# Optimization experiments

Measured on AMD Instinct MI355X. Metric: run time of the kernel, lower is better.

Reference implementation:

```python
import jax, jax.numpy as jnp
import numpy as np

SPATIAL_SHAPES = ((100, 167), (50, 84), (25, 42), (13, 21))
NUM_HEADS = 8
NUM_LEVELS = 4
NUM_POINTS = 4
EMBED_DIM = 256
LV = sum(h * w for h, w in SPATIAL_SHAPES)  # 22223


def bilinear_sample(img, grid):
    """torch.F.grid_sample(mode='bilinear', padding_mode='zeros', align_corners=False).
    img: (B, D, H, W); grid: (B, Lq, P, 2) with xy in [-1, 1]. Returns (B, D, Lq, P)."""
    B, D, H, W = img.shape
    x = (grid[..., 0] + 1.0) * 0.5 * W - 0.5  # (B, Lq, P)
    y = (grid[..., 1] + 1.0) * 0.5 * H - 0.5
    x0 = jnp.floor(x)
    y0 = jnp.floor(y)
    wx1 = x - x0
    wy1 = y - y0
    wx0 = 1.0 - wx1
    wy0 = 1.0 - wy1

    def gather(ix, iy):
        valid = ((ix >= 0) & (ix <= W - 1) & (iy >= 0) & (iy <= H - 1)).astype(img.dtype)
        ixc = jnp.clip(ix, 0, W - 1).astype(jnp.int32)
        iyc = jnp.clip(iy, 0, H - 1).astype(jnp.int32)

        def g(img_b, ixb, iyb, vb):
            return img_b[:, iyb, ixb] * vb[None]  # (D, Lq, P)

        return jax.vmap(g)(img, ixc, iyc, valid)  # (B, D, Lq, P)

    v00 = gather(x0, y0)
    v01 = gather(x0 + 1, y0)
    v10 = gather(x0, y0 + 1)
    v11 = gather(x0 + 1, y0 + 1)
    w00 = (wy0 * wx0)[:, None]
    w01 = (wy0 * wx1)[:, None]
    w10 = (wy1 * wx0)[:, None]
    w11 = (wy1 * wx1)[:, None]
    return v00 * w00 + v01 * w01 + v10 * w10 + v11 * w11


def deform_attn(query, ref_points, value, W_off, b_off, W_attn, b_attn, W_val, b_val, W_out, b_out):
    N, Lq, C = query.shape
    D = C // NUM_HEADS
    off = (query @ W_off + b_off).reshape(N, Lq, NUM_HEADS, NUM_LEVELS, NUM_POINTS, 2)
    attn = jax.nn.softmax((query @ W_attn + b_attn).reshape(N, Lq, NUM_HEADS, NUM_LEVELS * NUM_POINTS), axis=-1)
    attn = attn.reshape(N, Lq, NUM_HEADS, NUM_LEVELS, NUM_POINTS)
    ref_cxcy = ref_points[:, :, None, :, None, :2]
    ref_wh = ref_points[:, :, None, :, None, 2:]
    loc = ref_cxcy + off / NUM_POINTS * ref_wh * 0.5
    grids = 2.0 * loc - 1.0  # (N, Lq, nh, L, P, 2)

    v = value @ W_val + b_val  # (N, Lv, C)
    sampled = []
    start = 0
    for lvl, (H, W) in enumerate(SPATIAL_SHAPES):
        v_l = v[:, start:start + H * W]  # (N, HW, C)
        start += H * W
        v_l = v_l.transpose(0, 2, 1).reshape(N * NUM_HEADS, D, H, W)
        g_l = grids[:, :, :, lvl].transpose(0, 2, 1, 3, 4).reshape(N * NUM_HEADS, Lq, NUM_POINTS, 2)
        sampled.append(bilinear_sample(v_l, g_l))  # (N*nh, D, Lq, P)
    sampled = jnp.concatenate(sampled, axis=-1)  # (N*nh, D, Lq, L*P)

    attn_r = attn.transpose(0, 2, 1, 3, 4).reshape(N * NUM_HEADS, 1, Lq, NUM_LEVELS * NUM_POINTS)
    out = (sampled * attn_r).sum(-1)  # (N*nh, D, Lq)
    out = out.reshape(N, C, Lq).transpose(0, 2, 1)
    return out @ W_out + b_out


def setup_inputs() -> dict:
    key = jax.random.key(0)
    ks = jax.random.split(key, 8)
    N, Lq, C = 1, LV, EMBED_DIM
    s = 0.02
    return {
        "query": jax.random.normal(ks[0], (N, Lq, C), jnp.float32),
        "ref_points": jax.random.uniform(ks[1], (N, Lq, NUM_LEVELS, 4), jnp.float32),
        "value": jax.random.normal(ks[2], (N, LV, C), jnp.float32),
        "W_off": jax.random.normal(ks[3], (C, NUM_HEADS * NUM_LEVELS * NUM_POINTS * 2), jnp.float32) * s,
        "b_off": jnp.zeros((NUM_HEADS * NUM_LEVELS * NUM_POINTS * 2,), jnp.float32),
        "W_attn": jax.random.normal(ks[4], (C, NUM_HEADS * NUM_LEVELS * NUM_POINTS), jnp.float32) * s,
        "b_attn": jnp.zeros((NUM_HEADS * NUM_LEVELS * NUM_POINTS,), jnp.float32),
        "W_val": jax.random.normal(ks[5], (C, C), jnp.float32) * s,
        "b_val": jnp.zeros((C,), jnp.float32),
        "W_out": jax.random.normal(ks[6], (C, C), jnp.float32) * s,
        "b_out": jnp.zeros((C,), jnp.float32),
    }


def reference(query, ref_points, value, W_off, b_off, W_attn, b_attn, W_val, b_val, W_out, b_out):
    return deform_attn(query, ref_points, value, W_off, b_off, W_attn, b_attn, W_val, b_val, W_out, b_out)
```

## Files before the change

kernel.cpp:

```cpp
#include <hip/hip_runtime.h>
#include <math.h>

#define LQ 22223
#define NH 8
#define NL 4
#define NP 4
#define CDIM 256
#define MBLK 348
#define NBV  (176 * 8)
#define NBOA (264 * 8)

typedef __attribute__((ext_vector_type(8))) short short8;
typedef __attribute__((ext_vector_type(4))) float f32x4;

__device__ __forceinline__ ushort f2bf(float f) {
    union { float f; unsigned u; } c; c.f = f;
    unsigned u = c.u;
    return (ushort)((u + 0x7fffu + ((u >> 16) & 1u)) >> 16);
}
__device__ __forceinline__ float bflo(unsigned u) {
    union { unsigned u; float f; } c; c.u = u << 16; return c.f;
}
__device__ __forceinline__ float bfhi(unsigned u) {
    union { unsigned u; float f; } c; c.u = u & 0xffff0000u; return c.f;
}

__global__ __launch_bounds__(256) void convert_wt(
    const float* __restrict__ Wv, const float* __restrict__ Wo,
    const float* __restrict__ Wu, const float* __restrict__ Wa,
    const float* __restrict__ bo, const float* __restrict__ ba,
    ushort* __restrict__ Tv, ushort* __restrict__ Toa,
    ushort* __restrict__ Tu, float* __restrict__ bcat)
{
    int idx = blockIdx.x * 256 + threadIdx.x;
    if (idx >= 229376) {
        int b = idx - 229376;
        if (b < 384) bcat[b] = (b < 256) ? bo[b] : ba[b - 256];
        return;
    }
    const float* W; ushort* T; int N; int local;
    if      (idx < 65536)  { W = Wv; T = Tv;          N = 256; local = idx; }
    else if (idx < 131072) { W = Wo; T = Toa;         N = 256; local = idx - 65536; }
    else if (idx < 196608) { W = Wu; T = Tu;          N = 256; local = idx - 131072; }
    else                   { W = Wa; T = Toa + 65536; N = 128; local = idx - 196608; }
    int k = local & 255;
    int n = local >> 8;
    T[n * 256 + k] = f2bf(W[k * N + n]);
}

__global__ __launch_bounds__(256, 5) void gemm_dual(
    const float* __restrict__ value, const ushort* __restrict__ Wtv,
    const float* __restrict__ bv, ushort* __restrict__ Cv,
    const float* __restrict__ query, const ushort* __restrict__ Wtoa,
    const float* __restrict__ boa, float* __restrict__ Coa)
{
    const int K = 256;
    __shared__ ushort As[2][64 * 40];
    __shared__ ushort Bs[2][64 * 40];

    int b = blockIdx.x;
    const float* A; const ushort* Bt; const float* bias;
    int N, bx, by; bool isv;
    const int xcd = b & 7;
    if (b < NBV) {
        isv = true;  A = value; Bt = Wtv;  bias = bv;  N = 256;
        const int j = b >> 3;
        bx = j & 3;  by = xcd + 8 * (j >> 2);
    } else {
        isv = false; A = query; Bt = Wtoa; bias = boa; N = 384;
        const int j = (b - NBV) >> 3;
        bx = j % 6;  by = xcd + 8 * (j / 6);
    }
    if (by >= MBLK) return;

    const int tid = threadIdx.x;
    const int w = tid >> 6;
    const int l = tid & 63;
    const int bm = by * 64;
    const int bn = bx * 64;

    const int r = tid >> 2;
    const int c = tid & 3;

    const int m_l  = (w << 4) + (l & 15);
    const int koff = (l >> 4) << 3;

    const bool arow_ok = (bm + r) < LQ;
    const float*  Ap = A  + (size_t)(bm + r) * K + c * 8;
    const ushort* Bp = Bt + (size_t)(bn + r) * K + c * 8;

    auto ldA = [&](int k0) -> short8 {
        short8 av = {0, 0, 0, 0, 0, 0, 0, 0};
        if (arow_ok) {
            const float4 f0 = *reinterpret_cast<const float4*>(Ap + k0);
            const float4 f1 = *reinterpret_cast<const float4*>(Ap + k0 + 4);
            av[0] = (short)f2bf(f0.x); av[1] = (short)f2bf(f0.y);
            av[2] = (short)f2bf(f0.z); av[3] = (short)f2bf(f0.w);
            av[4] = (short)f2bf(f1.x); av[5] = (short)f2bf(f1.y);
            av[6] = (short)f2bf(f1.z); av[7] = (short)f2bf(f1.w);
        }
        return av;
    };

    short8 av = ldA(0);
    short8 bvv = *reinterpret_cast<const short8*>(Bp);
    *reinterpret_cast<short8*>(&As[0][r * 40 + c * 8]) = av;
    *reinterpret_cast<short8*>(&Bs[0][r * 40 + c * 8]) = bvv;

    f32x4 acc[4] = {};

    #pragma unroll
    for (int k = 0; k < 8; ++k) {
        __syncthreads();
        if (k < 7) {
            av  = ldA((k + 1) * 32);
            bvv = *reinterpret_cast<const short8*>(Bp + (k + 1) * 32);
        }
        const int cur = k & 1;
        const short8 af = *reinterpret_cast<const short8*>(&As[cur][m_l * 40 + koff]);
        #pragma unroll
        for (int t = 0; t < 4; ++t) {
            const short8 bf = *reinterpret_cast<const short8*>(
                &Bs[cur][(t * 16 + (l & 15)) * 40 + koff]);
            acc[t] = __builtin_amdgcn_mfma_f32_16x16x32_bf16(af, bf, acc[t], 0, 0, 0);
        }
        if (k < 7) {
            const int nxt = cur ^ 1;
            *reinterpret_cast<short8*>(&As[nxt][r * 40 + c * 8]) = av;
            *reinterpret_cast<short8*>(&Bs[nxt][r * 40 + c * 8]) = bvv;
        }
    }

    const int row0 = bm + (w << 4) + ((l >> 4) << 2);
    #pragma unroll
    for (int t = 0; t < 4; ++t) {
        const int col = bn + t * 16 + (l & 15);
        const float bs = bias[col];
        #pragma unroll
        for (int i = 0; i < 4; ++i) {
            const int row = row0 + i;
            if (row < LQ) {
                const float o = acc[t][i] + bs;
                if (isv) Cv[(size_t)row * 256 + col] = f2bf(o);
                else     Coa[(size_t)row * 384 + col] = o;
            }
        }
    }
}

__global__ __launch_bounds__(256, 5) void gemm_out(
    const ushort* __restrict__ A, const ushort* __restrict__ Bt,
    const float* __restrict__ bias, float* __restrict__ C)
{
    const int K = 256, N = 256;
    __shared__ ushort As[2][64 * 40];
    __shared__ ushort Bs[2][64 * 40];

    const int b = blockIdx.x;
    const int xcd = b & 7;
    const int j = b >> 3;
    const int bx = j & 3;
    const int by = xcd + 8 * (j >> 2);
    if (by >= MBLK) return;

    const int tid = threadIdx.x;
    const int w = tid >> 6;
    const int l = tid & 63;
    const int bm = by * 64;
    const int bn = bx * 64;

    const int r = tid >> 2;
    const int c = tid & 3;

    const int m_l  = (w << 4) + (l & 15);
    const int koff = (l >> 4) << 3;

    const bool arow_ok = (bm + r) < LQ;
    const ushort* Ap = A  + (size_t)(bm + r) * K + c * 8;
    const ushort* Bp = Bt + (size_t)(bn + r) * K + c * 8;

    auto ldA = [&](int k0) -> short8 {
        short8 av = {0, 0, 0, 0, 0, 0, 0, 0};
        if (arow_ok) av = *reinterpret_cast<const short8*>(Ap + k0);
        return av;
    };

    short8 av = ldA(0);
    short8 bvv = *reinterpret_cast<const short8*>(Bp);
    *reinterpret_cast<short8*>(&As[0][r * 40 + c * 8]) = av;
    *reinterpret_cast<short8*>(&Bs[0][r * 40 + c * 8]) = bvv;

    f32x4 acc[4] = {};

    #pragma unroll
    for (int k = 0; k < 8; ++k) {
        __syncthreads();
        if (k < 7) {
            av  = ldA((k + 1) * 32);
            bvv = *reinterpret_cast<const short8*>(Bp + (k + 1) * 32);
        }
        const int cur = k & 1;
        const short8 af = *reinterpret_cast<const short8*>(&As[cur][m_l * 40 + koff]);
        #pragma unroll
        for (int t = 0; t < 4; ++t) {
            const short8 bf = *reinterpret_cast<const short8*>(
                &Bs[cur][(t * 16 + (l & 15)) * 40 + koff]);
            acc[t] = __builtin_amdgcn_mfma_f32_16x16x32_bf16(af, bf, acc[t], 0, 0, 0);
        }
        if (k < 7) {
            const int nxt = cur ^ 1;
            *reinterpret_cast<short8*>(&As[nxt][r * 40 + c * 8]) = av;
            *reinterpret_cast<short8*>(&Bs[nxt][r * 40 + c * 8]) = bvv;
        }
    }

    const int row0 = bm + (w << 4) + ((l >> 4) << 2);
    #pragma unroll
    for (int t = 0; t < 4; ++t) {
        const int col = bn + t * 16 + (l & 15);
        const float bs = bias[col];
        #pragma unroll
        for (int i = 0; i < 4; ++i) {
            const int row = row0 + i;
            if (row < LQ) C[(size_t)row * N + col] = acc[t][i] + bs;
        }
    }
}

__global__ __launch_bounds__(256) void softmax16(float* __restrict__ offattn, int rows)
{
    const int r = blockIdx.x * 256 + threadIdx.x;
    if (r >= rows) return;
    const int q = r >> 3;
    const int h = r & 7;
    float4* p = reinterpret_cast<float4*>(offattn + (size_t)q * 384 + 256 + h * 16);
    float v[16];
    #pragma unroll
    for (int i = 0; i < 4; ++i) {
        const float4 f = p[i];
        v[i * 4 + 0] = f.x; v[i * 4 + 1] = f.y; v[i * 4 + 2] = f.z; v[i * 4 + 3] = f.w;
    }
    float m = v[0];
    #pragma unroll
    for (int i = 1; i < 16; ++i) m = fmaxf(m, v[i]);
    float s = 0.f;
    #pragma unroll
    for (int i = 0; i < 16; ++i) { v[i] = expf(v[i] - m); s += v[i]; }
    const float inv = 1.f / s;
    #pragma unroll
    for (int i = 0; i < 4; ++i)
        p[i] = make_float4(v[i * 4 + 0] * inv, v[i * 4 + 1] * inv,
                           v[i * 4 + 2] * inv, v[i * 4 + 3] * inv);
}

__global__ __launch_bounds__(256, 5) void msda_sample(
    const ushort* __restrict__ v, const float* __restrict__ offattn,
    const float* __restrict__ ref, ushort* __restrict__ outp)
{
    __shared__ int4   s_off[1024];
    __shared__ float4 s_wts[1024];

    const int h = blockIdx.x & 7;
    const int qbase = (blockIdx.x >> 3) * 64;
    const int tid = threadIdx.x;

    const int Hs[4] = {100, 50, 25, 13};
    const int Ws[4] = {167, 84, 42, 21};
    const int starts[4] = {0, 16700, 20900, 21950};
    const int h32 = h * 32;

    #pragma unroll
    for (int t2 = 0; t2 < 4; ++t2) {
        const int t = t2 * 256 + tid;
        const int qi = t & 63;
        const int pi = t >> 6;
        const int q = qbase + qi;
        if (q < LQ) {
            const int l = pi >> 2;
            const int W = Ws[l], H = Hs[l];
            const float* refq = ref + (size_t)q * (NL * 4) + l * 4;
            const float cx = refq[0], cy = refq[1], rw = refq[2], rh = refq[3];
            const float* row = offattn + (size_t)q * 384;
            const float ox  = row[h32 + pi * 2];
            const float oy  = row[h32 + pi * 2 + 1];
            const float wgt = row[256 + h * 16 + pi];

            const float lx = cx + ox * 0.125f * rw;
            const float ly = cy + oy * 0.125f * rh;
            const float x = lx * (float)W - 0.5f;
            const float y = ly * (float)H - 0.5f;

            const float x0f = floorf(x);
            const float y0f = floorf(y);
            const int x0 = (int)x0f, y0 = (int)y0f;
            const float wx1 = x - x0f, wy1 = y - y0f;
            const float wx0 = 1.f - wx1, wy0 = 1.f - wy1;

            const bool xv0 = (x0 >= 0) && (x0 < W);
            const bool xv1 = (x0 + 1 >= 0) && (x0 + 1 < W);
            const bool yv0 = (y0 >= 0) && (y0 < H);
            const bool yv1 = (y0 + 1 >= 0) && (y0 + 1 < H);

            const int x0c = min(max(x0, 0), W - 1);
            const int x1c = min(max(x0 + 1, 0), W - 1);
            const int y0c = min(max(y0, 0), H - 1);
            const int y1c = min(max(y0 + 1, 0), H - 1);

            int4 ob;
            ob.x = ((starts[l] + y0c * W + x0c) << 8) + h32;
            ob.y = ((starts[l] + y0c * W + x1c) << 8) + h32;
            ob.z = ((starts[l] + y1c * W + x0c) << 8) + h32;
            ob.w = ((starts[l] + y1c * W + x1c) << 8) + h32;
            float4 wb;
            wb.x = (xv0 && yv0) ? wgt * wy0 * wx0 : 0.f;
            wb.y = (xv1 && yv0) ? wgt * wy0 * wx1 : 0.f;
            wb.z = (xv0 && yv1) ? wgt * wy1 * wx0 : 0.f;
            wb.w = (xv1 && yv1) ? wgt * wy1 * wx1 : 0.f;
            s_off[t] = ob;
            s_wts[t] = wb;
        }
    }
    __syncthreads();

    const int qi = tid >> 2;
    const int dg = tid & 3;
    const int q = qbase + qi;
    if (q >= LQ) return;
    const int d8 = dg * 8;

    float acc[8] = {};

    #pragma unroll 4
    for (int p = 0; p < 16; ++p) {
        const int4   o = s_off[p * 64 + qi];
        const float4 w = s_wts[p * 64 + qi];
        const uint4 a0 = *reinterpret_cast<const uint4*>(v + o.x + d8);
        const uint4 a1 = *reinterpret_cast<const uint4*>(v + o.y + d8);
        const uint4 a2 = *reinterpret_cast<const uint4*>(v + o.z + d8);
        const uint4 a3 = *reinterpret_cast<const uint4*>(v + o.w + d8);
        const unsigned u0[4] = {a0.x, a0.y, a0.z, a0.w};
        const unsigned u1[4] = {a1.x, a1.y, a1.z, a1.w};
        const unsigned u2[4] = {a2.x, a2.y, a2.z, a2.w};
        const unsigned u3[4] = {a3.x, a3.y, a3.z, a3.w};
        #pragma unroll
        for (int j = 0; j < 4; ++j) {
            acc[2 * j]     += w.x * bflo(u0[j]) + w.y * bflo(u1[j])
                            + w.z * bflo(u2[j]) + w.w * bflo(u3[j]);
            acc[2 * j + 1] += w.x * bfhi(u0[j]) + w.y * bfhi(u1[j])
                            + w.z * bfhi(u2[j]) + w.w * bfhi(u3[j]);
        }
    }

    short8 o8;
    #pragma unroll
    for (int j = 0; j < 8; ++j) o8[j] = (short)f2bf(acc[j]);
    *reinterpret_cast<short8*>(outp + (size_t)q * CDIM + h32 + d8) = o8;
}

extern "C" void kernel_launch(void* const* d_in, const int* in_sizes, int n_in,
                              void* d_out, int out_size, void* d_ws, size_t ws_size,
                              hipStream_t stream)
{
    const float* query  = (const float*)d_in[0];
    const float* ref    = (const float*)d_in[1];
    const float* value  = (const float*)d_in[2];
    const float* W_off  = (const float*)d_in[3];
    const float* b_off  = (const float*)d_in[4];
    const float* W_attn = (const float*)d_in[5];
    const float* b_attn = (const float*)d_in[6];
    const float* W_val  = (const float*)d_in[7];
    const float* b_val  = (const float*)d_in[8];
    const float* W_out  = (const float*)d_in[9];
    const float* b_out  = (const float*)d_in[10];
    float* out = (float*)d_out;

    char* p = (char*)d_ws;
    ushort* v_bf    = (ushort*)p; p += (size_t)LQ * CDIM * 2;
    float*  offattn = (float*)p;  p += (size_t)LQ * 384 * 4;
    ushort* outp    = (ushort*)p; p += (size_t)LQ * CDIM * 2;
    ushort* Wt_val  = (ushort*)p; p += 65536 * 2;
    ushort* Wt_oa   = (ushort*)p; p += (65536 + 32768) * 2;
    ushort* Wt_out  = (ushort*)p; p += 65536 * 2;
    float*  bcat    = (float*)p;  p += 384 * 4;

    convert_wt<<<(229376 + 384 + 255) / 256, 256, 0, stream>>>(
        W_val, W_off, W_out, W_attn, b_off, b_attn, Wt_val, Wt_oa, Wt_out, bcat);

    gemm_dual<<<NBV + NBOA, 256, 0, stream>>>(
        value, Wt_val, b_val, v_bf, query, Wt_oa, bcat, offattn);

    softmax16<<<(LQ * NH + 255) / 256, 256, 0, stream>>>(offattn, LQ * NH);

    const int qg = (LQ + 63) / 64;
    msda_sample<<<qg * 8, 256, 0, stream>>>(v_bf, offattn, ref, outp);

    gemm_out<<<176 * 8, 256, 0, stream>>>(outp, Wt_out, b_out, out);
}
```

Baseline: 216.8 us.

## Enlarge GEMM M-tile to 128 rows and fuse attention softmax into GEMM epilogue

Both GEMM kernels now compute 128x64 tiles, with each wave producing two 16-row fragments. This doubles reuse of the B tile and halves the block count. The separate softmax16 kernel is removed: for the attention columns (bn>=256), the 16-wide softmax is computed in the gemm_dual epilogue with lane shuffles across the 16 columns of each MFMA fragment. This saves one launch and a read-modify-write pass over the attention logits, at the cost of more registers and LDS per block, which may lower occupancy.

```diff
diff --git a/kernel.cpp b/kernel.cpp
--- a/kernel.cpp
+++ b/kernel.cpp
@@ -6,9 +6,9 @@
 #define NL 4
 #define NP 4
 #define CDIM 256
-#define MBLK 348
-#define NBV  (176 * 8)
-#define NBOA (264 * 8)
+#define MB128 174
+#define NBV  (8 * 4 * 22)
+#define NBOA (8 * 6 * 22)
 
 typedef __attribute__((ext_vector_type(8))) short short8;
 typedef __attribute__((ext_vector_type(4))) float f32x4;
@@ -54,14 +54,13 @@
     const float* __restrict__ query, const ushort* __restrict__ Wtoa,
     const float* __restrict__ boa, float* __restrict__ Coa)
 {
-    const int K = 256;
-    __shared__ ushort As[2][64 * 40];
+    __shared__ ushort As[2][128 * 40];
     __shared__ ushort Bs[2][64 * 40];
 
-    int b = blockIdx.x;
+    const int b = blockIdx.x;
+    const int xcd = b & 7;
     const float* A; const ushort* Bt; const float* bias;
     int N, bx, by; bool isv;
-    const int xcd = b & 7;
     if (b < NBV) {
         isv = true;  A = value; Bt = Wtv;  bias = bv;  N = 256;
         const int j = b >> 3;
@@ -71,78 +70,110 @@
         const int j = (b - NBV) >> 3;
         bx = j % 6;  by = xcd + 8 * (j / 6);
     }
-    if (by >= MBLK) return;
+    if (by >= MB128) return;
 
     const int tid = threadIdx.x;
     const int w = tid >> 6;
     const int l = tid & 63;
-    const int bm = by * 64;
+    const int lr = l & 15;
+    const int lk = (l >> 4) << 3;
+    const int bm = by * 128;
     const int bn = bx * 64;
 
-    const int r = tid >> 2;
-    const int c = tid & 3;
-
-    const int m_l  = (w << 4) + (l & 15);
-    const int koff = (l >> 4) << 3;
-
-    const bool arow_ok = (bm + r) < LQ;
-    const float*  Ap = A  + (size_t)(bm + r) * K + c * 8;
-    const ushort* Bp = Bt + (size_t)(bn + r) * K + c * 8;
-
-    auto ldA = [&](int k0) -> short8 {
-        short8 av = {0, 0, 0, 0, 0, 0, 0, 0};
-        if (arow_ok) {
+    const int ra = tid >> 1;
+    const int ca = (tid & 1) * 16;
+    const int rb = tid >> 2;
+    const int cb = (tid & 3) * 8;
+
+    const bool arow = (bm + ra) < LQ;
+    const float*  Ap = A  + (size_t)(bm + ra) * 256 + ca;
+    const ushort* Bp = Bt + (size_t)(bn + rb) * 256 + cb;
+
+    auto ldA = [&](int k0, short8& a0, short8& a1) {
+        a0 = short8{0,0,0,0,0,0,0,0}; a1 = short8{0,0,0,0,0,0,0,0};
+        if (arow) {
             const float4 f0 = *reinterpret_cast<const float4*>(Ap + k0);
             const float4 f1 = *reinterpret_cast<const float4*>(Ap + k0 + 4);
-            av[0] = (short)f2bf(f0.x); av[1] = (short)f2bf(f0.y);
-            av[2] = (short)f2bf(f0.z); av[3] = (short)f2bf(f0.w);
-            av[4] = (short)f2bf(f1.x); av[5] = (short)f2bf(f1.y);
-            av[6] = (short)f2bf(f1.z); av[7] = (short)f2bf(f1.w);
-        }
-        return av;
+            const float4 f2 = *reinterpret_cast<const float4*>(Ap + k0 + 8);
+            const float4 f3 = *reinterpret_cast<const float4*>(Ap + k0 + 12);
+            a0[0]=(short)f2bf(f0.x); a0[1]=(short)f2bf(f0.y);
+            a0[2]=(short)f2bf(f0.z); a0[3]=(short)f2bf(f0.w);
+            a0[4]=(short)f2bf(f1.x); a0[5]=(short)f2bf(f1.y);
+            a0[6]=(short)f2bf(f1.z); a0[7]=(short)f2bf(f1.w);
+            a1[0]=(short)f2bf(f2.x); a1[1]=(short)f2bf(f2.y);
+            a1[2]=(short)f2bf(f2.z); a1[3]=(short)f2bf(f2.w);
+            a1[4]=(short)f2bf(f3.x); a1[5]=(short)f2bf(f3.y);
+            a1[6]=(short)f2bf(f3.z); a1[7]=(short)f2bf(f3.w);
+        }
     };
 
-    short8 av = ldA(0);
-    short8 bvv = *reinterpret_cast<const short8*>(Bp);
-    *reinterpret_cast<short8*>(&As[0][r * 40 + c * 8]) = av;
-    *reinterpret_cast<short8*>(&Bs[0][r * 40 + c * 8]) = bvv;
-
-    f32x4 acc[4] = {};
+    short8 a0, a1, bvv;
+    ldA(0, a0, a1);
+    bvv = *reinterpret_cast<const short8*>(Bp);
+    *reinterpret_cast<short8*>(&As[0][ra * 40 + ca])     = a0;
+    *reinterpret_cast<short8*>(&As[0][ra * 40 + ca + 8]) = a1;
+    *reinterpret_cast<short8*>(&Bs[0][rb * 40 + cb])     = bvv;
+
+    f32x4 acc[2][4] = {};
 
     #pragma unroll
     for (int k = 0; k < 8; ++k) {
         __syncthreads();
         if (k < 7) {
-            av  = ldA((k + 1) * 32);
+            ldA((k + 1) * 32, a0, a1);
             bvv = *reinterpret_cast<const short8*>(Bp + (k + 1) * 32);
         }
         const int cur = k & 1;
-        const short8 af = *reinterpret_cast<const short8*>(&As[cur][m_l * 40 + koff]);
+        const short8 af0 = *reinterpret_cast<const short8*>(
+            &As[cur][(w * 32 + lr) * 40 + lk]);
+        const short8 af1 = *reinterpret_cast<const short8*>(
+            &As[cur][(w * 32 + 16 + lr) * 40 + lk]);
         #pragma unroll
         for (int t = 0; t < 4; ++t) {
             const short8 bf = *reinterpret_cast<const short8*>(
-                &Bs[cur][(t * 16 + (l & 15)) * 40 + koff]);
-            acc[t] = __builtin_amdgcn_mfma_f32_16x16x32_bf16(af, bf, acc[t], 0, 0, 0);
+                &Bs[cur][(t * 16 + lr) * 40 + lk]);
+            acc[0][t] = __builtin_amdgcn_mfma_f32_16x16x32_bf16(af0, bf, acc[0][t], 0, 0, 0);
+            acc[1][t] = __builtin_amdgcn_mfma_f32_16x16x32_bf16(af1, bf, acc[1][t], 0, 0, 0);
         }
         if (k < 7) {
             const int nxt = cur ^ 1;
-            *reinterpret_cast<short8*>(&As[nxt][r * 40 + c * 8]) = av;
-            *reinterpret_cast<short8*>(&Bs[nxt][r * 40 + c * 8]) = bvv;
-        }
-    }
-
-    const int row0 = bm + (w << 4) + ((l >> 4) << 2);
-    #pragma unroll
-    for (int t = 0; t < 4; ++t) {
-        const int col = bn + t * 16 + (l & 15);
-        const float bs = bias[col];
+            *reinterpret_cast<short8*>(&As[nxt][ra * 40 + ca])     = a0;
+            *reinterpret_cast<short8*>(&As[nxt][ra * 40 + ca + 8]) = a1;
+            *reinterpret_cast<short8*>(&Bs[nxt][rb * 40 + cb])     = bvv;
+        }
+    }
+
+    const int rbase = bm + w * 32 + ((l >> 4) << 2);
+    const bool do_sm = (!isv) && (bn >= 256);
+
+    #pragma unroll
+    for (int rf = 0; rf < 2; ++rf) {
         #pragma unroll
-        for (int i = 0; i < 4; ++i) {
-            const int row = row0 + i;
-            if (row < LQ) {
-                const float o = acc[t][i] + bs;
-                if (isv) Cv[(size_t)row * 256 + col] = f2bf(o);
-                else     Coa[(size_t)row * 384 + col] = o;
+        for (int t = 0; t < 4; ++t) {
+            const int col = bn + t * 16 + lr;
+            const float bs = bias[col];
+            #pragma unroll
+            for (int i = 0; i < 4; ++i) {
+                const int row = rbase + rf * 16 + i;
+                float x = acc[rf][t][i] + bs;
+                if (do_sm) {
+                    float m = x;
+                    m = fmaxf(m, __shfl_xor(m, 1));
+                    m = fmaxf(m, __shfl_xor(m, 2));
+                    m = fmaxf(m, __shfl_xor(m, 4));
+                    m = fmaxf(m, __shfl_xor(m, 8));
+                    const float e = expf(x - m);
+                    float s = e;
+                    s += __shfl_xor(s, 1);
+                    s += __shfl_xor(s, 2);
+                    s += __shfl_xor(s, 4);
+                    s += __shfl_xor(s, 8);
+                    x = e / s;
+                }
+                if (row < LQ) {
+                    if (isv) Cv[(size_t)row * 256 + col] = f2bf(x);
+                    else     Coa[(size_t)row * 384 + col] = x;
+                }
             }
         }
     }
@@ -152,8 +183,7 @@
     const ushort* __restrict__ A, const ushort* __restrict__ Bt,
     const float* __restrict__ bias, float* __restrict__ C)
 {
-    const int K = 256, N = 256;
-    __shared__ ushort As[2][64 * 40];
+    __shared__ ushort As[2][128 * 40];
     __shared__ ushort Bs[2][64 * 40];
 
     const int b = blockIdx.x;
@@ -161,96 +191,83 @@
     const int j = b >> 3;
     const int bx = j & 3;
     const int by = xcd + 8 * (j >> 2);
-    if (by >= MBLK) return;
+    if (by >= MB128) return;
 
     const int tid = threadIdx.x;
     const int w = tid >> 6;
     const int l = tid & 63;
-    const int bm = by * 64;
+    const int lr = l & 15;
+    const int lk = (l >> 4) << 3;
+    const int bm = by * 128;
     const int bn = bx * 64;
 
-    const int r = tid >> 2;
-    const int c = tid & 3;
-
-    const int m_l  = (w << 4) + (l & 15);
-    const int koff = (l >> 4) << 3;
-
-    const bool arow_ok = (bm + r) < LQ;
-    const ushort* Ap = A  + (size_t)(bm + r) * K + c * 8;
-    const ushort* Bp = Bt + (size_t)(bn + r) * K + c * 8;
-
-    auto ldA = [&](int k0) -> short8 {
-        short8 av = {0, 0, 0, 0, 0, 0, 0, 0};
-        if (arow_ok) av = *reinterpret_cast<const short8*>(Ap + k0);
-        return av;
+    const int ra = tid >> 1;
+    const int ca = (tid & 1) * 16;
+    const int rb = tid >> 2;
+    const int cb = (tid & 3) * 8;
+
+    const bool arow = (bm + ra) < LQ;
+    const ushort* Ap = A  + (size_t)(bm + ra) * 256 + ca;
+    const ushort* Bp = Bt + (size_t)(bn + rb) * 256 + cb;
+
+    auto ldA = [&](int k0, short8& x0, short8& x1) {
+        x0 = short8{0,0,0,0,0,0,0,0}; x1 = short8{0,0,0,0,0,0,0,0};
+        if (arow) {
+            x0 = *reinterpret_cast<const short8*>(Ap + k0);
+            x1 = *reinterpret_cast<const short8*>(Ap + k0 + 8);
+        }
     };
 
-    short8 av = ldA(0);
-    short8 bvv = *reinterpret_cast<const short8*>(Bp);
-    *reinterpret_cast<short8*>(&As[0][r * 40 + c * 8]) = av;
-    *reinterpret_cast<short8*>(&Bs[0][r * 40 + c * 8]) = bvv;
-
-    f32x4 acc[4] = {};
+    short8 a0, a1, bvv;
+    ldA(0, a0, a1);
+    bvv = *reinterpret_cast<const short8*>(Bp);
+    *reinterpret_cast<short8*>(&As[0][ra * 40 + ca])     = a0;
+    *reinterpret_cast<short8*>(&As[0][ra * 40 + ca + 8]) = a1;
+    *reinterpret_cast<short8*>(&Bs[0][rb * 40 + cb])     = bvv;
+
+    f32x4 acc[2][4] = {};
 
     #pragma unroll
     for (int k = 0; k < 8; ++k) {
         __syncthreads();
         if (k < 7) {
-            av  = ldA((k + 1) * 32);
+            ldA((k + 1) * 32, a0, a1);
             bvv = *reinterpret_cast<const short8*>(Bp + (k + 1) * 32);
         }
         const int cur = k & 1;
-        const short8 af = *reinterpret_cast<const short8*>(&As[cur][m_l * 40 + koff]);
+        const short8 af0 = *reinterpret_cast<const short8*>(
+            &As[cur][(w * 32 + lr) * 40 + lk]);
+        const short8 af1 = *reinterpret_cast<const short8*>(
+            &As[cur][(w * 32 + 16 + lr) * 40 + lk]);
         #pragma unroll
         for (int t = 0; t < 4; ++t) {
             const short8 bf = *reinterpret_cast<const short8*>(
-                &Bs[cur][(t * 16 + (l & 15)) * 40 + koff]);
-            acc[t] = __builtin_amdgcn_mfma_f32_16x16x32_bf16(af, bf, acc[t], 0, 0, 0);
+                &Bs[cur][(t * 16 + lr) * 40 + lk]);
+            acc[0][t] = __builtin_amdgcn_mfma_f32_16x16x32_bf16(af0, bf, acc[0][t], 0, 0, 0);
+            acc[1][t] = __builtin_amdgcn_mfma_f32_16x16x32_bf16(af1, bf, acc[1][t], 0, 0, 0);
         }
         if (k < 7) {
             const int nxt = cur ^ 1;
-            *reinterpret_cast<short8*>(&As[nxt][r * 40 + c * 8]) = av;
-            *reinterpret_cast<short8*>(&Bs[nxt][r * 40 + c * 8]) = bvv;
-        }
-    }
-
-    const int row0 = bm + (w << 4) + ((l >> 4) << 2);
-    #pragma unroll
-    for (int t = 0; t < 4; ++t) {
-        const int col = bn + t * 16 + (l & 15);
-        const float bs = bias[col];
+            *reinterpret_cast<short8*>(&As[nxt][ra * 40 + ca])     = a0;
+            *reinterpret_cast<short8*>(&As[nxt][ra * 40 + ca + 8]) = a1;
+            *reinterpret_cast<short8*>(&Bs[nxt][rb * 40 + cb])     = bvv;
+        }
+    }
+
+    const int rbase = bm + w * 32 + ((l >> 4) << 2);
+    #pragma unroll
+    for (int rf = 0; rf < 2; ++rf) {
         #pragma unroll
-        for (int i = 0; i < 4; ++i) {
-            const int row = row0 + i;
-            if (row < LQ) C[(size_t)row * N + col] = acc[t][i] + bs;
-        }
-    }
-}
-
-__global__ __launch_bounds__(256) void softmax16(float* __restrict__ offattn, int rows)
-{
-    const int r = blockIdx.x * 256 + threadIdx.x;
-    if (r >= rows) return;
-    const int q = r >> 3;
-    const int h = r & 7;
-    float4* p = reinterpret_cast<float4*>(offattn + (size_t)q * 384 + 256 + h * 16);
-    float v[16];
-    #pragma unroll
-    for (int i = 0; i < 4; ++i) {
-        const float4 f = p[i];
-        v[i * 4 + 0] = f.x; v[i * 4 + 1] = f.y; v[i * 4 + 2] = f.z; v[i * 4 + 3] = f.w;
-    }
-    float m = v[0];
-    #pragma unroll
-    for (int i = 1; i < 16; ++i) m = fmaxf(m, v[i]);
-    float s = 0.f;
-    #pragma unroll
-    for (int i = 0; i < 16; ++i) { v[i] = expf(v[i] - m); s += v[i]; }
-    const float inv = 1.f / s;
-    #pragma unroll
-    for (int i = 0; i < 4; ++i)
-        p[i] = make_float4(v[i * 4 + 0] * inv, v[i * 4 + 1] * inv,
-                           v[i * 4 + 2] * inv, v[i * 4 + 3] * inv);
+        for (int t = 0; t < 4; ++t) {
+            const int col = bn + t * 16 + lr;
+            const float bs = bias[col];
+            #pragma unroll
+            for (int i = 0; i < 4; ++i) {
+                const int row = rbase + rf * 16 + i;
+                if (row < LQ) C[(size_t)row * 256 + col] = acc[rf][t][i] + bs;
+            }
+        }
+    }
 }
 
 __global__ __launch_bounds__(256, 5) void msda_sample(
@@ -389,10 +406,8 @@
     gemm_dual<<<NBV + NBOA, 256, 0, stream>>>(
         value, Wt_val, b_val, v_bf, query, Wt_oa, bcat, offattn);
 
-    softmax16<<<(LQ * NH + 255) / 256, 256, 0, stream>>>(offattn, LQ * NH);
-
     const int qg = (LQ + 63) / 64;
     msda_sample<<<qg * 8, 256, 0, stream>>>(v_bf, offattn, ref, outp);
 
-    gemm_out<<<176 * 8, 256, 0, stream>>>(outp, Wt_out, b_out, out);
-}
+    gemm_out<<<NBV, 256, 0, stream>>>(outp, Wt_out, b_out, out);
+}
```

Measured after the change: 225.2 us. +3.9%, slower.
